# Kernel optimization log

Hardware: AMD Instinct MI355X
Metric: run time of the kernel (lower is better)

## Reference

```python
import jax, jax.numpy as jnp
import numpy as np

HEADS = 16
DIM_HEAD = 64
SCALE = DIM_HEAD ** -0.5


def setup_inputs() -> dict:
    key = jax.random.key(0)
    k1, k2, k3 = jax.random.split(key, 3)
    B, N, C = 2, 2048, 1024
    inner = HEADS * DIM_HEAD  # 1024
    x = jax.random.normal(k1, (B, N, C), dtype=jnp.float32)
    w_qkv = jax.random.normal(k2, (C, 3 * inner), dtype=jnp.float32) * (C ** -0.5)
    w_proj = jax.random.normal(k3, (inner, C), dtype=jnp.float32) * (inner ** -0.5)
    b_proj = jnp.zeros((C,), dtype=jnp.float32)
    return {"x": x, "w_qkv": w_qkv, "w_proj": w_proj, "b_proj": b_proj}


def reference(x, w_qkv, w_proj, b_proj):
    B, N, C = x.shape
    qkv = x @ w_qkv  # [B, N, 3*inner]
    qkv = qkv.reshape(B, N, 3, HEADS, DIM_HEAD)
    qkv = jnp.transpose(qkv, (2, 0, 3, 1, 4))  # [3, B, H, N, D]
    q, k, v = qkv[0], qkv[1], qkv[2]
    q = q * SCALE
    attn = jnp.einsum('bhnd,bhmd->bhnm', q, k)  # [B, H, N, N]
    attn = jax.nn.softmax(attn, axis=-1)
    out = jnp.einsum('bhnm,bhmd->bhnd', attn, v)  # [B, H, N, D]
    out = jnp.transpose(out, (0, 2, 1, 3)).reshape(B, N, HEADS * DIM_HEAD)
    return out @ w_proj + b_proj
```

## Files before the change

### kernel.cpp

```cpp
#include <hip/hip_runtime.h>
#include <hip/hip_bf16.h>
#include <cstdint>
#include <cstddef>

static constexpr int BATCH = 2;
static constexpr int SEQ   = 2048;
static constexpr int CDIM  = 1024;
static constexpr int ROWS  = BATCH * SEQ;
static constexpr int QKVN  = 3 * CDIM;
static constexpr int QKN   = 2 * CDIM;

typedef short bf16x8 __attribute__((ext_vector_type(8)));
typedef short bf16x4 __attribute__((ext_vector_type(4)));
typedef float f32x4  __attribute__((ext_vector_type(4)));

__device__ inline short f2bf(float f) {
    union { float f; unsigned u; } v; v.f = f;
    unsigned u = v.u;
    u += 0x7fffu + ((u >> 16) & 1u);
    return (short)(u >> 16);
}

__device__ inline unsigned pk_bf16(float a, float b) {
#if __has_builtin(__builtin_amdgcn_cvt_pk_bf16_f32)
    auto r = __builtin_amdgcn_cvt_pk_bf16_f32(a, b);
    return __builtin_bit_cast(unsigned, r);
#else
    union { float f; unsigned u; } ua, ub;
    ua.f = a; ub.f = b;
    unsigned xa = ua.u + 0x7fffu + ((ua.u >> 16) & 1u);
    unsigned xb = ub.u + 0x7fffu + ((ub.u >> 16) & 1u);
    return __builtin_amdgcn_perm(xb, xa, 0x07060302);
#endif
}

__device__ inline void glds16(const short* g, short* l) {
    __builtin_amdgcn_global_load_lds(
        (const __attribute__((address_space(1))) void*)g,
        (__attribute__((address_space(3))) void*)l, 16, 0, 0);
}

__device__ inline f32x4 mfma16_bf16(bf16x4 a, bf16x4 b, f32x4 c) {
#if __has_builtin(__builtin_amdgcn_mfma_f32_16x16x16bf16_1k)
    return __builtin_amdgcn_mfma_f32_16x16x16bf16_1k(a, b, c, 0, 0, 0);
#else
    asm("v_mfma_f32_16x16x16_bf16 %0, %1, %2, %0" : "+v"(c) : "v"(a), "v"(b));
    return c;
#endif
}

__device__ inline int swz_src(int lane) {
    return ((lane & 3) ^ ((lane >> 3) & 3)) * 8;
}
__device__ inline int swz_rd(int quad, int l15) {
    return (quad ^ ((l15 >> 1) & 3)) * 8;
}

__global__ __launch_bounds__(256) void prep(const float* __restrict__ x,
                                            const float* __restrict__ wqkv,
                                            const float* __restrict__ wproj,
                                            short* __restrict__ x_bf,
                                            short* __restrict__ wqkvT,
                                            short* __restrict__ wprojT,
                                            float smul) {
    __shared__ float tile[32][33];
    const int bid = blockIdx.x, t = threadIdx.x;
    if (bid < 4096) {
        int i = bid * 256 + t;
        float4 f = ((const float4*)x)[i];
        uint2 o;
        o.x = pk_bf16(f.x, f.y);
        o.y = pk_bf16(f.z, f.w);
        ((uint2*)x_bf)[i] = o;
        return;
    }
    const float* in; short* out; int C, r0, c0; float scale; int srows;
    if (bid < 7168) {
        int b2 = bid - 4096;
        in = wqkv; out = wqkvT; C = QKVN;
        c0 = (b2 % 96) * 32; r0 = (b2 / 96) * 32;
        scale = smul; srows = 1024;
    } else {
        int b3 = bid - 7168;
        in = wproj; out = wprojT; C = CDIM;
        c0 = (b3 & 31) * 32; r0 = (b3 >> 5) * 32;
        scale = 1.0f; srows = 0;
    }
    int tx = t & 31, ty = t >> 5;
    #pragma unroll
    for (int i = 0; i < 4; i++)
        tile[ty + i * 8][tx] = in[(size_t)(r0 + ty + i * 8) * C + c0 + tx];
    __syncthreads();
    #pragma unroll
    for (int i = 0; i < 4; i++) {
        int orow = c0 + ty + i * 8;
        float sc = (orow < srows) ? scale : 1.0f;
        out[(size_t)orow * CDIM + r0 + tx] = f2bf(tile[tx][ty + i * 8] * sc);
    }
}

template<int BF16OUT, int MT>
__device__ __forceinline__ void gemm_core(const short* __restrict__ A,
                                          const short* __restrict__ Bt,
                                          void* __restrict__ C,
                                          const float* __restrict__ bias,
                                          int N, int K, int m0, int n0,
                                          short* As, short* Bs) {
    constexpr int AF = MT / 32;
    constexpr int APAN = MT * 32;
    constexpr int BPAN = 128 * 32;
    const int t = threadIdx.x, wave = t >> 6, lane = t & 63;
    const int l15 = lane & 15, quad = lane >> 4;
    const int wr = wave >> 1, wc = wave & 1;
    const int sg = swz_src(lane);
    const int rsl = swz_rd(quad, l15);

    f32x4 acc[AF][4] = {};

    const short* gA = A  + (size_t)(m0 + wave * (MT / 4) + (lane >> 2)) * K + sg;
    const short* gB = Bt + (size_t)(n0 + wave * 32 + (lane >> 2)) * K + sg;
    short* lA = &As[wave * (MT / 4) * 32];
    short* lB = &Bs[wave * 32 * 32];

    for (int k0 = 0; k0 < K; k0 += 64) {
        glds16(gA + k0,      lA);
        glds16(gA + k0 + 32, lA + APAN);
        if constexpr (MT == 128) {
            glds16(gA + 16 * K + k0,      lA + 512);
            glds16(gA + 16 * K + k0 + 32, lA + APAN + 512);
        }
        glds16(gB + k0,               lB);
        glds16(gB + 16 * K + k0,      lB + 512);
        glds16(gB + k0 + 32,          lB + BPAN);
        glds16(gB + 16 * K + k0 + 32, lB + BPAN + 512);
        __syncthreads();

        #pragma unroll
        for (int st = 0; st < 2; st++) {
            bf16x8 af[AF], bfv[4];
            #pragma unroll
            for (int i = 0; i < AF; i++)
                af[i] = *(const bf16x8*)&As[st * APAN + (wr * (MT / 2) + i * 16 + l15) * 32 + rsl];
            #pragma unroll
            for (int j = 0; j < 4; j++)
                bfv[j] = *(const bf16x8*)&Bs[st * BPAN + (wc * 64 + j * 16 + l15) * 32 + rsl];
            #pragma unroll
            for (int i = 0; i < AF; i++)
                #pragma unroll
                for (int j = 0; j < 4; j++)
                    acc[i][j] = __builtin_amdgcn_mfma_f32_16x16x32_bf16(af[i], bfv[j], acc[i][j], 0, 0, 0);
        }
        __syncthreads();
    }

    #pragma unroll
    for (int i = 0; i < AF; i++) {
        #pragma unroll
        for (int j = 0; j < 4; j++) {
            #pragma unroll
            for (int r = 0; r < 4; r++) {
                int row = m0 + wr * (MT / 2) + i * 16 + quad * 4 + r;
                int col = n0 + wc * 64 + j * 16 + l15;
                float v = acc[i][j][r];
                if (BF16OUT) ((short*)C)[(size_t)row * N + col] = f2bf(v);
                else         ((float*)C)[(size_t)row * N + col] = v + bias[col];
            }
        }
    }
}

__global__ __launch_bounds__(256) void gemm_qk_v(const short* __restrict__ x_bf,
                                                 const short* __restrict__ wqkvT,
                                                 short* __restrict__ qk,
                                                 short* __restrict__ vT) {
    __shared__ __align__(16) short As[128 * 64];
    __shared__ __align__(16) short Bs[128 * 64];
    const int bid = blockIdx.x;
    if (bid < 512) {
        const int c = bid & 7, i = bid >> 3;
        const int mi = i & 7, ni = i >> 3;
        const int m0 = ((c & 3) * 8 + mi) * 128;
        const int n0 = ((c >> 2) * 8 + ni) * 128;
        gemm_core<1, 128>(x_bf, wqkvT, qk, nullptr, QKN, CDIM, m0, n0, As, Bs);
    } else {
        const int b2 = bid - 512;
        const int c = b2 & 7, i = b2 >> 3;
        const int mi = i & 3, ni = i >> 2;
        const int m0 = ((c & 1) * 4 + mi) * 128;
        const int n0 = ((c >> 1) * 8 + ni) * 128;
        gemm_core<1, 128>(wqkvT + (size_t)QKN * CDIM, x_bf, vT, nullptr, ROWS, CDIM,
                          m0, n0, As, Bs);
    }
}

__global__ __launch_bounds__(256) void gemm_proj(const short* __restrict__ A,
                                                 const short* __restrict__ Bt,
                                                 float* __restrict__ C,
                                                 const float* __restrict__ bias) {
    __shared__ __align__(16) short As[64 * 64];
    __shared__ __align__(16) short Bs[128 * 64];
    const int bid = blockIdx.x;
    const int c = bid & 7, i = bid >> 3;
    const int mi = i & 7, ni = i >> 3;
    const int m0 = (c * 8 + mi) * 64;
    const int n0 = ni * 128;
    gemm_core<0, 64>(A, Bt, C, bias, CDIM, CDIM, m0, n0, As, Bs);
}

static constexpr int KBUF  = 2 * 128 * 32;
static constexpr int VOFF  = 2 * KBUF;
static constexpr int LDV   = 136;
static constexpr int VBUF  = 64 * LDV;
static constexpr int SMEM_SH = 26624;

__global__ __launch_bounds__(512) void attn_kernel(const short* __restrict__ qk,
                                                   const short* __restrict__ vTg,
                                                   short* __restrict__ attn_out) {
    __shared__ __align__(16) short smem[SMEM_SH];

    const int t = threadIdx.x, wave = t >> 6, lane = t & 63;
    const int l15 = lane & 15, quad = lane >> 4;
    const int g = wave >> 2, wl = wave & 3;
    const int lid = blockIdx.x;
    const int bh = (lid & 7) * 4 + (lid >> 7);
    const int q0 = ((lid >> 3) & 15) * 128;
    const int b = bh >> 4, h = bh & 15;
    const size_t baseQ = (size_t)(b * SEQ) * QKN + h * 64;
    const int rsl = swz_rd(quad, l15);

    const size_t qoff0 = baseQ + (size_t)(q0 + wl * 32 + l15) * QKN + quad * 8;
    const size_t qoff1 = qoff0 + (size_t)16 * QKN;
    bf16x8 qf00 = *(const bf16x8*)&qk[qoff0];
    bf16x8 qf01 = *(const bf16x8*)&qk[qoff0 + 32];
    bf16x8 qf10 = *(const bf16x8*)&qk[qoff1];
    bf16x8 qf11 = *(const bf16x8*)&qk[qoff1 + 32];

    const short* gK = qk + baseQ + 1024
                    + (size_t)(wave * 16 + (lane >> 2)) * QKN + swz_src(lane);
    const short* gV = vTg + (size_t)(h * 64) * ROWS + b * SEQ;
    const int vd = t >> 3, vc = t & 7;

    const bf16x4 ones = { (short)0x3F80, (short)0x3F80, (short)0x3F80, (short)0x3F80 };

    f32x4 ot0[4] = {}, ot1[4] = {};
    f32x4 ol0 = {}, ol1 = {};

    short* Vbuf = smem + VOFF;

    glds16(gK,      smem + wave * 512);
    glds16(gK + 32, smem + 4096 + wave * 512);
    {
        int4 va = *(const int4*)&gV[(size_t)vd * ROWS + vc * 8];
        int4 vb = *(const int4*)&gV[(size_t)vd * ROWS + 64 + vc * 8];
        *(int4*)&Vbuf[vd * LDV + vc * 8]      = va;
        *(int4*)&Vbuf[vd * LDV + 64 + vc * 8] = vb;
    }
    __syncthreads();

    for (int j = 0; j < SEQ / 128; j++) {
        int4 va, vb;
        if (j < SEQ / 128 - 1) {
            const size_t jadd = (size_t)(j + 1) * 128 * QKN;
            short* kb = smem + ((j + 1) & 1) * KBUF + wave * 512;
            glds16(gK + jadd,      kb);
            glds16(gK + jadd + 32, kb + 4096);
            va = *(const int4*)&gV[(size_t)vd * ROWS + (j + 1) * 128 + vc * 8];
            vb = *(const int4*)&gV[(size_t)vd * ROWS + (j + 1) * 128 + 64 + vc * 8];
        }

        const short* Kb0 = smem + (j & 1) * KBUF;
        const short* Kb1 = Kb0 + 4096;

        #pragma unroll
        for (int sub = 0; sub < 4; sub++) {
            const int gsub = g * 4 + sub;
            bf16x8 kf0 = *(const bf16x8*)&Kb0[(gsub * 16 + l15) * 32 + rsl];
            bf16x8 kf1 = *(const bf16x8*)&Kb1[(gsub * 16 + l15) * 32 + rsl];
            f32x4 a0 = {}, a1 = {};
            __builtin_amdgcn_s_setprio(1);
            a0 = __builtin_amdgcn_mfma_f32_16x16x32_bf16(kf0, qf00, a0, 0, 0, 0);
            a0 = __builtin_amdgcn_mfma_f32_16x16x32_bf16(kf1, qf01, a0, 0, 0, 0);
            a1 = __builtin_amdgcn_mfma_f32_16x16x32_bf16(kf0, qf10, a1, 0, 0, 0);
            a1 = __builtin_amdgcn_mfma_f32_16x16x32_bf16(kf1, qf11, a1, 0, 0, 0);
            __builtin_amdgcn_s_setprio(0);
            union { unsigned u[2]; bf16x4 v; } pu0, pu1;
            pu0.u[0] = pk_bf16(__builtin_amdgcn_exp2f(a0[0]), __builtin_amdgcn_exp2f(a0[1]));
            pu0.u[1] = pk_bf16(__builtin_amdgcn_exp2f(a0[2]), __builtin_amdgcn_exp2f(a0[3]));
            pu1.u[0] = pk_bf16(__builtin_amdgcn_exp2f(a1[0]), __builtin_amdgcn_exp2f(a1[1]));
            pu1.u[1] = pk_bf16(__builtin_amdgcn_exp2f(a1[2]), __builtin_amdgcn_exp2f(a1[3]));
            __builtin_amdgcn_s_setprio(1);
            ol0 = mfma16_bf16(ones, pu0.v, ol0);
            ol1 = mfma16_bf16(ones, pu1.v, ol1);
            #pragma unroll
            for (int d = 0; d < 4; d++) {
                bf16x4 vf = *(const bf16x4*)&Vbuf[(d * 16 + l15) * LDV + gsub * 16 + quad * 4];
                ot0[d] = mfma16_bf16(vf, pu0.v, ot0[d]);
                ot1[d] = mfma16_bf16(vf, pu1.v, ot1[d]);
            }
            __builtin_amdgcn_s_setprio(0);
        }

        __syncthreads();
        if (j < SEQ / 128 - 1) {
            *(int4*)&Vbuf[vd * LDV + vc * 8]      = va;
            *(int4*)&Vbuf[vd * LDV + 64 + vc * 8] = vb;
            __syncthreads();
        }
    }

    __syncthreads();
    float* pf = (float*)smem;
    short* tr = smem + 17408;

    if (g == 1) {
        #pragma unroll
        for (int d = 0; d < 4; d++) {
            #pragma unroll
            for (int r = 0; r < 4; r++) {
                pf[(wl * 32 + l15) * 68      + d * 16 + quad * 4 + r] = ot0[d][r];
                pf[(wl * 32 + 16 + l15) * 68 + d * 16 + quad * 4 + r] = ot1[d][r];
            }
        }
        pf[(wl * 32 + l15) * 68 + 64]      = ol0[0];
        pf[(wl * 32 + 16 + l15) * 68 + 64] = ol1[0];
    }
    __syncthreads();
    if (g == 0) {
        float inv0 = 1.0f / (ol0[0] + pf[(wl * 32 + l15) * 68 + 64]);
        float inv1 = 1.0f / (ol1[0] + pf[(wl * 32 + 16 + l15) * 68 + 64]);
        #pragma unroll
        for (int d = 0; d < 4; d++) {
            int pb0 = (wl * 32 + l15) * 68      + d * 16 + quad * 4;
            int pb1 = (wl * 32 + 16 + l15) * 68 + d * 16 + quad * 4;
            float c00 = (ot0[d][0] + pf[pb0 + 0]) * inv0;
            float c01 = (ot0[d][1] + pf[pb0 + 1]) * inv0;
            float c02 = (ot0[d][2] + pf[pb0 + 2]) * inv0;
            float c03 = (ot0[d][3] + pf[pb0 + 3]) * inv0;
            float c10 = (ot1[d][0] + pf[pb1 + 0]) * inv1;
            float c11 = (ot1[d][1] + pf[pb1 + 1]) * inv1;
            float c12 = (ot1[d][2] + pf[pb1 + 2]) * inv1;
            float c13 = (ot1[d][3] + pf[pb1 + 3]) * inv1;
            int o0 = (wl * 32 + l15) * 72 + d * 16 + quad * 4;
            int o1 = (wl * 32 + 16 + l15) * 72 + d * 16 + quad * 4;
            *(unsigned*)&tr[o0]     = pk_bf16(c00, c01);
            *(unsigned*)&tr[o0 + 2] = pk_bf16(c02, c03);
            *(unsigned*)&tr[o1]     = pk_bf16(c10, c11);
            *(unsigned*)&tr[o1 + 2] = pk_bf16(c12, c13);
        }
    }
    __syncthreads();
    {
        int row = t >> 2, c4 = t & 3;
        #pragma unroll
        for (int p = 0; p < 2; p++) {
            int ch = c4 * 2 + p;
            int4 v = *(const int4*)&tr[row * 72 + ch * 8];
            *(int4*)&attn_out[(size_t)(b * SEQ + q0 + row) * CDIM + h * 64 + ch * 8] = v;
        }
    }
}

extern "C" void kernel_launch(void* const* d_in, const int* in_sizes, int n_in,
                              void* d_out, int out_size, void* d_ws, size_t ws_size,
                              hipStream_t stream) {
    const float* x      = (const float*)d_in[0];
    const float* w_qkv  = (const float*)d_in[1];
    const float* w_proj = (const float*)d_in[2];
    const float* b_proj = (const float*)d_in[3];
    float* out = (float*)d_out;

    char* ws = (char*)d_ws;
    short* x_bf    = (short*)(ws);
    short* wqkvT   = (short*)(ws + 8388608);
    short* wprojT  = (short*)(ws + 14680064);
    short* qk_bf   = (short*)(ws + 16777216);
    short* vTg     = (short*)(ws + 33554432);
    short* attn_bf = (short*)(ws + 41943040);

    const float SMUL = 0.125f * 1.44269504088896340736f;

    prep<<<8192, 256, 0, stream>>>(x, w_qkv, w_proj, x_bf, wqkvT, wprojT, SMUL);

    gemm_qk_v<<<768, 256, 0, stream>>>(x_bf, wqkvT, qk_bf, vTg);

    attn_kernel<<<dim3(512), 512, 0, stream>>>(qk_bf, vTg, attn_bf);

    gemm_proj<<<512, 256, 0, stream>>>(attn_bf, wprojT, out, b_proj);
}
```

Measured before the change: 181.7 us.

## Triple-buffer GEMM LDS staging with explicit vmcnt waits to overlap loads

Replaces the single-buffered 64-wide K loop in the shared GEMM core with a three-stage ring of 32-wide K slices. Loads for step s+2 are issued before computing step s, and explicit s_waitcnt vmcnt counts wait only for the oldest slice. This hides global-to-LDS latency behind MFMA work instead of stalling at each iteration. It adds barriers per 32-K step, 1.5x LDS footprint, and relies on hand-counted vmcnt values matching the number of issued loads.

```diff
diff --git a/kernel.cpp b/kernel.cpp
--- a/kernel.cpp
+++ b/kernel.cpp
@@ -119,38 +119,53 @@
 
     const short* gA = A  + (size_t)(m0 + wave * (MT / 4) + (lane >> 2)) * K + sg;
     const short* gB = Bt + (size_t)(n0 + wave * 32 + (lane >> 2)) * K + sg;
-    short* lA = &As[wave * (MT / 4) * 32];
-    short* lB = &Bs[wave * 32 * 32];
-
-    for (int k0 = 0; k0 < K; k0 += 64) {
-        glds16(gA + k0,      lA);
-        glds16(gA + k0 + 32, lA + APAN);
-        if constexpr (MT == 128) {
-            glds16(gA + 16 * K + k0,      lA + 512);
-            glds16(gA + 16 * K + k0 + 32, lA + APAN + 512);
-        }
-        glds16(gB + k0,               lB);
-        glds16(gB + 16 * K + k0,      lB + 512);
-        glds16(gB + k0 + 32,          lB + BPAN);
-        glds16(gB + 16 * K + k0 + 32, lB + BPAN + 512);
-        __syncthreads();
-
-        #pragma unroll
-        for (int st = 0; st < 2; st++) {
-            bf16x8 af[AF], bfv[4];
-            #pragma unroll
-            for (int i = 0; i < AF; i++)
-                af[i] = *(const bf16x8*)&As[st * APAN + (wr * (MT / 2) + i * 16 + l15) * 32 + rsl];
+
+    auto STAGE = [&](int buf, int k) {
+        short* a = As + buf * APAN + wave * (MT / 4) * 32;
+        short* b = Bs + buf * BPAN + wave * 32 * 32;
+        glds16(gA + k, a);
+        if constexpr (MT == 128) glds16(gA + 16 * K + k, a + 512);
+        glds16(gB + k,          b);
+        glds16(gB + 16 * K + k, b + 512);
+    };
+
+    const int NSTEP = K / 32;
+    STAGE(0, 0);
+    STAGE(1, 32);
+
+    for (int s = 0; s < NSTEP; s++) {
+        const int cur = s % 3;
+        if (s + 2 < NSTEP) {
+            STAGE((s + 2) % 3, (s + 2) * 32);
+            if constexpr (MT == 128)
+                asm volatile("s_waitcnt vmcnt(8)" ::: "memory");
+            else
+                asm volatile("s_waitcnt vmcnt(6)" ::: "memory");
+        } else if (s + 1 < NSTEP) {
+            if constexpr (MT == 128)
+                asm volatile("s_waitcnt vmcnt(4)" ::: "memory");
+            else
+                asm volatile("s_waitcnt vmcnt(3)" ::: "memory");
+        } else {
+            asm volatile("s_waitcnt vmcnt(0)" ::: "memory");
+        }
+        __builtin_amdgcn_s_barrier();
+
+        bf16x8 af[AF], bfv[4];
+        #pragma unroll
+        for (int i = 0; i < AF; i++)
+            af[i] = *(const bf16x8*)&As[cur * APAN + (wr * (MT / 2) + i * 16 + l15) * 32 + rsl];
+        #pragma unroll
+        for (int j = 0; j < 4; j++)
+            bfv[j] = *(const bf16x8*)&Bs[cur * BPAN + (wc * 64 + j * 16 + l15) * 32 + rsl];
+        #pragma unroll
+        for (int i = 0; i < AF; i++)
             #pragma unroll
             for (int j = 0; j < 4; j++)
-                bfv[j] = *(const bf16x8*)&Bs[st * BPAN + (wc * 64 + j * 16 + l15) * 32 + rsl];
-            #pragma unroll
-            for (int i = 0; i < AF; i++)
-                #pragma unroll
-                for (int j = 0; j < 4; j++)
-                    acc[i][j] = __builtin_amdgcn_mfma_f32_16x16x32_bf16(af[i], bfv[j], acc[i][j], 0, 0, 0);
-        }
-        __syncthreads();
+                acc[i][j] = __builtin_amdgcn_mfma_f32_16x16x32_bf16(af[i], bfv[j], acc[i][j], 0, 0, 0);
+
+        asm volatile("s_waitcnt lgkmcnt(0)" ::: "memory");
+        __builtin_amdgcn_s_barrier();
     }
 
     #pragma unroll
@@ -173,8 +188,8 @@
                                                  const short* __restrict__ wqkvT,
                                                  short* __restrict__ qk,
                                                  short* __restrict__ vT) {
-    __shared__ __align__(16) short As[128 * 64];
-    __shared__ __align__(16) short Bs[128 * 64];
+    __shared__ __align__(16) short As[3 * 128 * 32];
+    __shared__ __align__(16) short Bs[3 * 128 * 32];
     const int bid = blockIdx.x;
     if (bid < 512) {
         const int c = bid & 7, i = bid >> 3;
@@ -197,8 +212,8 @@
                                                  const short* __restrict__ Bt,
                                                  float* __restrict__ C,
                                                  const float* __restrict__ bias) {
-    __shared__ __align__(16) short As[64 * 64];
-    __shared__ __align__(16) short Bs[128 * 64];
+    __shared__ __align__(16) short As[3 * 64 * 32];
+    __shared__ __align__(16) short Bs[3 * 128 * 32];
     const int bid = blockIdx.x;
     const int c = bid & 7, i = bid >> 3;
     const int mi = i & 7, ni = i >> 3;
```

Measured after the change: 194.8 us. 7.2% more time.
